# Kernel tuning notes

Measured on AMD Instinct MI355X. Metric: run time of the kernel, lower is better.

Reference implementation:

```python
import jax, jax.numpy as jnp
import numpy as np

N_HEAD = 12

def setup_inputs() -> dict:
    key = jax.random.key(0)
    k1, k2, k3 = jax.random.split(key, 3)
    B, T, C = 8, 1024, 768
    x = jax.random.normal(k1, (B, T, C), dtype=jnp.float32)
    # Linear weights stored as [in, out] so y = x @ W + b (same math as torch Linear)
    w_attn = jax.random.normal(k2, (C, 3 * C), dtype=jnp.float32) * (1.0 / np.sqrt(C))
    b_attn = jnp.zeros((3 * C,), dtype=jnp.float32)
    w_proj = jax.random.normal(k3, (C, C), dtype=jnp.float32) * (1.0 / np.sqrt(C))
    b_proj = jnp.zeros((C,), dtype=jnp.float32)
    return {"x": x, "w_attn": w_attn, "b_attn": b_attn, "w_proj": w_proj, "b_proj": b_proj}

def reference(x, w_attn, b_attn, w_proj, b_proj):
    B, T, C = x.shape
    H = N_HEAD
    D = C // H
    qkv = x @ w_attn + b_attn                        # [B,T,3C]
    q, k, v = jnp.split(qkv, 3, axis=-1)             # each [B,T,C]
    q = q.reshape(B, T, H, D).transpose(0, 2, 1, 3)  # [B,H,T,D]
    k = k.reshape(B, T, H, D).transpose(0, 2, 1, 3)
    v = v.reshape(B, T, H, D).transpose(0, 2, 1, 3)
    scale = 1.0 / jnp.sqrt(jnp.asarray(D, dtype=x.dtype))
    att = jnp.einsum('bhqd,bhkd->bhqk', q, k) * scale  # [B,H,T,T]
    causal = jnp.tril(jnp.ones((T, T), dtype=bool))    # [T,T]
    att = jnp.where(causal[None, None], att, jnp.asarray(-jnp.inf, dtype=att.dtype))
    att = jax.nn.softmax(att, axis=-1)
    out = jnp.einsum('bhqk,bhkd->bhqd', att, v)        # [B,H,T,D]
    out = out.transpose(0, 2, 1, 3).reshape(B, T, C)
    return out @ w_proj + b_proj
```

## Files before the change

kernel.cpp:

```cpp
#include <hip/hip_runtime.h>
#include <hip/hip_bf16.h>
#include <cmath>

#define B_ 8
#define T_ 1024
#define C_ 768
#define H_ 12
#define D_ 64
#define N3C 2304
#define M_ 8192

typedef __bf16 bf16x8 __attribute__((ext_vector_type(8)));
typedef float  f32x4  __attribute__((ext_vector_type(4)));

typedef const __attribute__((address_space(1))) void* gptr_t;
typedef __attribute__((address_space(3))) void* lptr_t;

#define LOG2E 1.44269504088896f

__device__ __forceinline__ bf16x8 cvt_bf16x8(const float4& a, const float4& b) {
    bf16x8 r;
    r[0] = (__bf16)a.x; r[1] = (__bf16)a.y; r[2] = (__bf16)a.z; r[3] = (__bf16)a.w;
    r[4] = (__bf16)b.x; r[5] = (__bf16)b.y; r[6] = (__bf16)b.z; r[7] = (__bf16)b.w;
    return r;
}

__global__ __launch_bounds__(256) void prepass(const float* __restrict__ x,
                                               __bf16* __restrict__ xb,
                                               const float* __restrict__ wa,
                                               __bf16* __restrict__ wat,
                                               const float* __restrict__ wp,
                                               __bf16* __restrict__ wpt) {
    __shared__ float tile[32][33];
    const int bx = blockIdx.x, tid = threadIdx.x;
    if (bx < 3072) {
        int i = (bx * 256 + tid) * 8;
        float4 a = *(const float4*)&x[i];
        float4 b = *(const float4*)&x[i + 4];
        *(bf16x8*)&xb[i] = cvt_bf16x8(a, b);
        return;
    }
    const float* w;
    __bf16* wt;
    int K, N, n0, k0;
    if (bx < 4800) {
        int bb = bx - 3072;
        w = wa; wt = wat; K = 768; N = 2304;
        n0 = (bb % 72) * 32; k0 = (bb / 72) * 32;
    } else {
        int bb = bx - 4800;
        w = wp; wt = wpt; K = 768; N = 768;
        n0 = (bb % 24) * 32; k0 = (bb / 24) * 32;
    }
    int tx = tid & 31, ty = tid >> 5;
#pragma unroll
    for (int i = 0; i < 4; i++)
        tile[ty + i * 8][tx] = w[(size_t)(k0 + ty + i * 8) * N + n0 + tx];
    __syncthreads();
#pragma unroll
    for (int i = 0; i < 4; i++)
        wt[(size_t)(n0 + ty + i * 8) * K + k0 + tx] = (__bf16)tile[tx][ty + i * 8];
}

__global__ __launch_bounds__(256) void qkv_gemm_mfma(const __bf16* __restrict__ A,
                                                     const __bf16* __restrict__ Bt,
                                                     const float* __restrict__ bias,
                                                     __bf16* __restrict__ qb,
                                                     __bf16* __restrict__ kb,
                                                     __bf16* __restrict__ vbt) {
    __shared__ __bf16 smem[128 * 136];
    __bf16* As = smem;
    __bf16* Bs = smem + 128 * 64;
    const int tid = threadIdx.x;
    const int wave = tid >> 6, lane = tid & 63;
    const int lane15 = lane & 15, quad = lane >> 4;
    const int bid = blockIdx.x;
    const int m0 = ((bid & 7) * 8 + ((bid >> 3) & 7)) * 128;
    const int n0 = (bid >> 6) * 128;
    const int wm = (wave >> 1) * 64, wn = (wave & 1) * 64;
    f32x4 acc[4][4] = {};

    for (int k0 = 0; k0 < 768; k0 += 64) {
#pragma unroll
        for (int r = 0; r < 4; ++r) {
            int p = r * 256 + tid;
            int mrow = p >> 3, csw = p & 7;
            int ksrc = (csw ^ (mrow & 7)) * 8;
            __builtin_amdgcn_global_load_lds(
                (gptr_t)(A + (size_t)(m0 + mrow) * 768 + k0 + ksrc),
                (lptr_t)(As + (r * 256 + wave * 64) * 8), 16, 0, 0);
            __builtin_amdgcn_global_load_lds(
                (gptr_t)(Bt + (size_t)(n0 + mrow) * 768 + k0 + ksrc),
                (lptr_t)(Bs + (r * 256 + wave * 64) * 8), 16, 0, 0);
        }
        __syncthreads();
#pragma unroll
        for (int ks = 0; ks < 2; ++ks) {
            bf16x8 af[4], bf[4];
#pragma unroll
            for (int mt = 0; mt < 4; ++mt) {
                int m = wm + mt * 16 + lane15;
                int csw = (ks * 4 + quad) ^ (m & 7);
                af[mt] = *(const bf16x8*)(As + m * 64 + csw * 8);
            }
#pragma unroll
            for (int nt = 0; nt < 4; ++nt) {
                int n = wn + nt * 16 + lane15;
                int csw = (ks * 4 + quad) ^ (n & 7);
                bf[nt] = *(const bf16x8*)(Bs + n * 64 + csw * 8);
            }
#pragma unroll
            for (int mt = 0; mt < 4; ++mt)
#pragma unroll
                for (int nt = 0; nt < 4; ++nt)
                    acc[mt][nt] = __builtin_amdgcn_mfma_f32_16x16x32_bf16(af[mt], bf[nt], acc[mt][nt], 0, 0, 0);
        }
        __syncthreads();
    }

    if (n0 < 1536) {
        const bool isq = (n0 < 768);
        const float sc = isq ? (0.125f * LOG2E) : 1.0f;
#pragma unroll
        for (int nt = 0; nt < 4; ++nt) {
            int n = n0 + wn + nt * 16 + lane15;
            int rem = isq ? n : (n - 768);
            int h = rem >> 6;
            int d = n & 63;
            float bv = bias[n];
            __bf16* dst = isq ? qb : kb;
#pragma unroll
            for (int mt = 0; mt < 4; ++mt) {
#pragma unroll
                for (int reg = 0; reg < 4; ++reg) {
                    int mr = m0 + wm + mt * 16 + quad * 4 + reg;
                    int bb = mr >> 10, t = mr & 1023;
                    dst[(((size_t)bb * H_ + h) * T_ + t) * D_ + d] =
                        (__bf16)((acc[mt][nt][reg] + bv) * sc);
                }
            }
        }
    } else {
        __bf16* vls = smem;
#pragma unroll
        for (int nt = 0; nt < 4; ++nt) {
            int nl = wn + nt * 16 + lane15;
            float bv = bias[n0 + nl];
#pragma unroll
            for (int mt = 0; mt < 4; ++mt)
#pragma unroll
                for (int reg = 0; reg < 4; ++reg)
                    vls[nl * 136 + wm + mt * 16 + quad * 4 + reg] =
                        (__bf16)(acc[mt][nt][reg] + bv);
        }
        __syncthreads();
        int nl = tid >> 1;
        int t0 = (tid & 1) * 64;
        int n = n0 + nl;
        int h = (n - 1536) >> 6;
        int d = n & 63;
        int bb = m0 >> 10, tg = (m0 & 1023) + t0;
        __bf16* dst = vbt + (((size_t)bb * H_ + h) * D_ + d) * T_ + tg;
        const __bf16* srcl = vls + nl * 136 + t0;
#pragma unroll
        for (int c = 0; c < 8; ++c)
            *(bf16x8*)(dst + c * 8) = *(const bf16x8*)(srcl + c * 8);
    }
}

__global__ __launch_bounds__(256) void proj_gemm_mfma(const __bf16* __restrict__ A,
                                                      const __bf16* __restrict__ Bt,
                                                      const float* __restrict__ bias,
                                                      float* __restrict__ out) {
    __shared__ __bf16 As[128 * 64];
    __shared__ __bf16 Bs[64 * 64];
    const int tid = threadIdx.x;
    const int wave = tid >> 6, lane = tid & 63;
    const int lane15 = lane & 15, quad = lane >> 4;
    const int bid = blockIdx.x;
    const int m0 = ((bid & 7) * 8 + ((bid >> 3) & 7)) * 128;
    const int n0 = (bid >> 6) * 64;
    const int wm = wave * 32;
    f32x4 acc[2][4] = {};

    for (int k0 = 0; k0 < 768; k0 += 64) {
#pragma unroll
        for (int r = 0; r < 4; ++r) {
            int p = r * 256 + tid;
            int mrow = p >> 3, csw = p & 7;
            int ksrc = (csw ^ (mrow & 7)) * 8;
            __builtin_amdgcn_global_load_lds(
                (gptr_t)(A + (size_t)(m0 + mrow) * 768 + k0 + ksrc),
                (lptr_t)(As + (r * 256 + wave * 64) * 8), 16, 0, 0);
        }
#pragma unroll
        for (int r = 0; r < 2; ++r) {
            int p = r * 256 + tid;
            int nrow = p >> 3, csw = p & 7;
            int ksrc = (csw ^ (nrow & 7)) * 8;
            __builtin_amdgcn_global_load_lds(
                (gptr_t)(Bt + (size_t)(n0 + nrow) * 768 + k0 + ksrc),
                (lptr_t)(Bs + (r * 256 + wave * 64) * 8), 16, 0, 0);
        }
        __syncthreads();
#pragma unroll
        for (int ks = 0; ks < 2; ++ks) {
            bf16x8 af[2], bf[4];
#pragma unroll
            for (int mt = 0; mt < 2; ++mt) {
                int m = wm + mt * 16 + lane15;
                int csw = (ks * 4 + quad) ^ (m & 7);
                af[mt] = *(const bf16x8*)(As + m * 64 + csw * 8);
            }
#pragma unroll
            for (int nt = 0; nt < 4; ++nt) {
                int n = nt * 16 + lane15;
                int csw = (ks * 4 + quad) ^ (n & 7);
                bf[nt] = *(const bf16x8*)(Bs + n * 64 + csw * 8);
            }
#pragma unroll
            for (int mt = 0; mt < 2; ++mt)
#pragma unroll
                for (int nt = 0; nt < 4; ++nt)
                    acc[mt][nt] = __builtin_amdgcn_mfma_f32_16x16x32_bf16(af[mt], bf[nt], acc[mt][nt], 0, 0, 0);
        }
        __syncthreads();
    }

#pragma unroll
    for (int nt = 0; nt < 4; ++nt) {
        int n = n0 + nt * 16 + lane15;
        float bv = bias[n];
#pragma unroll
        for (int mt = 0; mt < 2; ++mt) {
#pragma unroll
            for (int reg = 0; reg < 4; ++reg) {
                int mr = m0 + wm + mt * 16 + quad * 4 + reg;
                out[(size_t)mr * C_ + n] = acc[mt][nt][reg] + bv;
            }
        }
    }
}

__global__ __launch_bounds__(256) void attn_mfma(const __bf16* __restrict__ qb,
                                                 const __bf16* __restrict__ kb,
                                                 const __bf16* __restrict__ vbt,
                                                 __bf16* __restrict__ ao) {
    __shared__ __bf16 Ks[2][64 * 64];
    __shared__ __bf16 Vts[2][64 * 64];
    __shared__ __bf16 Ps[4 * 32 * 72];

    const int tid = threadIdx.x;
    const int wave = tid >> 6, lane = tid & 63;
    const int lane15 = lane & 15, quad = lane >> 4;
    const int bh = blockIdx.x;
    const int qt = 7 - blockIdx.y;
    const int b = bh / H_, h = bh % H_;
    const int q0 = qt * 128;

    const __bf16* Kb = kb + (size_t)bh * T_ * D_;
    const __bf16* Vb = vbt + (size_t)bh * D_ * T_;
    __bf16* Pw = Ps + wave * 32 * 72;

    bf16x8 qf[2][2];
#pragma unroll
    for (int g = 0; g < 2; ++g) {
        const __bf16* qrow = qb + ((size_t)bh * T_ + q0 + wave * 32 + g * 16 + lane15) * D_ + quad * 8;
        qf[g][0] = *(const bf16x8*)qrow;
        qf[g][1] = *(const bf16x8*)(qrow + 32);
    }

    f32x4 o[2][4] = {};
    float lsum[2][4] = {};

    const int kunits = 2 * qt + 2;

#define STAGE(KU, BUF)                                                             \
    {                                                                              \
        const int k0s = (KU) * 64;                                                 \
        _Pragma("unroll")                                                          \
        for (int r = 0; r < 2; ++r) {                                              \
            int p = r * 256 + tid;                                                 \
            int row = p >> 3, c = p & 7;                                           \
            int cs = (c ^ (row & 7)) * 8;                                          \
            __builtin_amdgcn_global_load_lds(                                      \
                (gptr_t)(Kb + (size_t)(k0s + row) * D_ + cs),                      \
                (lptr_t)(&Ks[BUF][0] + (r * 256 + wave * 64) * 8), 16, 0, 0);      \
            __builtin_amdgcn_global_load_lds(                                      \
                (gptr_t)(Vb + (size_t)row * T_ + k0s + cs),                        \
                (lptr_t)(&Vts[BUF][0] + (r * 256 + wave * 64) * 8), 16, 0, 0);     \
        }                                                                          \
    }

    STAGE(0, 0);

    for (int ku = 0; ku < kunits; ++ku) {
        __syncthreads();
        if (ku + 1 < kunits) STAGE(ku + 1, (ku + 1) & 1);
        const __bf16* Kc = &Ks[ku & 1][0];
        const __bf16* Vc = &Vts[ku & 1][0];
        const int k0 = ku * 64;

        f32x4 s[2][4];
#pragma unroll
        for (int kt = 0; kt < 4; ++kt) {
            int row = kt * 16 + lane15;
            bf16x8 kf0 = *(const bf16x8*)(Kc + row * 64 + ((quad) ^ (row & 7)) * 8);
            bf16x8 kf1 = *(const bf16x8*)(Kc + row * 64 + ((4 + quad) ^ (row & 7)) * 8);
#pragma unroll
            for (int g = 0; g < 2; ++g) {
                f32x4 t = {};
                t = __builtin_amdgcn_mfma_f32_16x16x32_bf16(qf[g][0], kf0, t, 0, 0, 0);
                t = __builtin_amdgcn_mfma_f32_16x16x32_bf16(qf[g][1], kf1, t, 0, 0, 0);
                s[g][kt] = t;
            }
        }

        const bool diag = (ku >= 2 * qt);
#pragma unroll
        for (int g = 0; g < 2; ++g) {
#pragma unroll
            for (int kt = 0; kt < 4; ++kt) {
                int col = k0 + kt * 16 + lane15;
#pragma unroll
                for (int r = 0; r < 4; ++r) {
                    float p = __builtin_amdgcn_exp2f(s[g][kt][r]);
                    if (diag) {
                        int qrow = q0 + wave * 32 + g * 16 + quad * 4 + r;
                        if (col > qrow) p = 0.f;
                    }
                    lsum[g][r] += p;
                    Pw[(g * 16 + quad * 4 + r) * 72 + kt * 16 + lane15] = (__bf16)p;
                }
            }
        }

        bf16x8 vf[4][2];
#pragma unroll
        for (int dt = 0; dt < 4; ++dt) {
            int row = dt * 16 + lane15;
#pragma unroll
            for (int half = 0; half < 2; ++half)
                vf[dt][half] = *(const bf16x8*)(Vc + row * 64 + ((half * 4 + quad) ^ (row & 7)) * 8);
        }
#pragma unroll
        for (int g = 0; g < 2; ++g) {
#pragma unroll
            for (int half = 0; half < 2; ++half) {
                bf16x8 pf = *(const bf16x8*)(Pw + (g * 16 + lane15) * 72 + half * 32 + quad * 8);
#pragma unroll
                for (int dt = 0; dt < 4; ++dt)
                    o[g][dt] = __builtin_amdgcn_mfma_f32_16x16x32_bf16(pf, vf[dt][half], o[g][dt], 0, 0, 0);
            }
        }
    }

#pragma unroll
    for (int g = 0; g < 2; ++g) {
        float inv[4];
#pragma unroll
        for (int r = 0; r < 4; ++r) {
            float ls = lsum[g][r];
            ls += __shfl_xor(ls, 1);
            ls += __shfl_xor(ls, 2);
            ls += __shfl_xor(ls, 4);
            ls += __shfl_xor(ls, 8);
            inv[r] = 1.0f / ls;
        }
#pragma unroll
        for (int dt = 0; dt < 4; ++dt) {
#pragma unroll
            for (int r = 0; r < 4; ++r) {
                int t = q0 + wave * 32 + g * 16 + quad * 4 + r;
                ao[((size_t)(b * T_ + t)) * C_ + h * 64 + dt * 16 + lane15] =
                    (__bf16)(o[g][dt][r] * inv[r]);
            }
        }
    }
}

extern "C" void kernel_launch(void* const* d_in, const int* in_sizes, int n_in,
                              void* d_out, int out_size, void* d_ws, size_t ws_size,
                              hipStream_t stream) {
    const float* x = (const float*)d_in[0];
    const float* w_attn = (const float*)d_in[1];
    const float* b_attn = (const float*)d_in[2];
    const float* w_proj = (const float*)d_in[3];
    const float* b_proj = (const float*)d_in[4];
    float* out = (float*)d_out;

    __bf16* xb = (__bf16*)d_ws;
    __bf16* wat = xb + (size_t)M_ * C_;
    __bf16* wpt = wat + (size_t)N3C * C_;
    __bf16* qb = wpt + (size_t)C_ * C_;
    __bf16* kb = qb + (size_t)96 * T_ * D_;
    __bf16* vbt = kb + (size_t)96 * T_ * D_;
    __bf16* ao = vbt + (size_t)96 * T_ * D_;

    prepass<<<5376, 256, 0, stream>>>(x, xb, w_attn, wat, w_proj, wpt);
    qkv_gemm_mfma<<<1152, 256, 0, stream>>>(xb, wat, b_attn, qb, kb, vbt);
    attn_mfma<<<dim3(96, 8), 256, 0, stream>>>(qb, kb, vbt, ao);
    proj_gemm_mfma<<<768, 256, 0, stream>>>(ao, wpt, b_proj, out);
}
```

Baseline: 188.9 us.

## Double-buffer GEMM K-loops and vectorize attention P stores via permuted V layout

The QKV and projection GEMMs now use two LDS buffers. The next K-chunk is prefetched with global_load_lds while the current one is computed, which drops one __syncthreads per iteration and hides global load latency. In attention, the per-element bf16 writes of P to LDS become one 4-wide vector store per row. That permutes the key order within each 64-key block, so the V-transpose epilogue of the QKV GEMM is changed to write V in the matching permuted order. The cost is double the LDS in the GEMMs, which may lower occupancy, and a scalar gather in the V epilogue.

```diff
diff --git a/kernel.cpp b/kernel.cpp
--- a/kernel.cpp
+++ b/kernel.cpp
@@ -10,6 +10,7 @@
 #define N3C 2304
 #define M_ 8192
 
+typedef __bf16 bf16x4 __attribute__((ext_vector_type(4)));
 typedef __bf16 bf16x8 __attribute__((ext_vector_type(8)));
 typedef float  f32x4  __attribute__((ext_vector_type(4)));
 
@@ -68,9 +69,7 @@
                                                      __bf16* __restrict__ qb,
                                                      __bf16* __restrict__ kb,
                                                      __bf16* __restrict__ vbt) {
-    __shared__ __bf16 smem[128 * 136];
-    __bf16* As = smem;
-    __bf16* Bs = smem + 128 * 64;
+    __shared__ __bf16 smem[2][2][128 * 64];
     const int tid = threadIdx.x;
     const int wave = tid >> 6, lane = tid & 63;
     const int lane15 = lane & 15, quad = lane >> 4;
@@ -80,20 +79,29 @@
     const int wm = (wave >> 1) * 64, wn = (wave & 1) * 64;
     f32x4 acc[4][4] = {};
 
-    for (int k0 = 0; k0 < 768; k0 += 64) {
-#pragma unroll
-        for (int r = 0; r < 4; ++r) {
-            int p = r * 256 + tid;
-            int mrow = p >> 3, csw = p & 7;
-            int ksrc = (csw ^ (mrow & 7)) * 8;
-            __builtin_amdgcn_global_load_lds(
-                (gptr_t)(A + (size_t)(m0 + mrow) * 768 + k0 + ksrc),
-                (lptr_t)(As + (r * 256 + wave * 64) * 8), 16, 0, 0);
-            __builtin_amdgcn_global_load_lds(
-                (gptr_t)(Bt + (size_t)(n0 + mrow) * 768 + k0 + ksrc),
-                (lptr_t)(Bs + (r * 256 + wave * 64) * 8), 16, 0, 0);
-        }
+#define QSTAGE(KC, BUF)                                                             \
+    {                                                                               \
+        const int k0s = (KC) * 64;                                                  \
+        _Pragma("unroll")                                                           \
+        for (int r = 0; r < 4; ++r) {                                               \
+            int p = r * 256 + tid;                                                  \
+            int mrow = p >> 3, csw = p & 7;                                         \
+            int ksrc = (csw ^ (mrow & 7)) * 8;                                      \
+            __builtin_amdgcn_global_load_lds(                                       \
+                (gptr_t)(A + (size_t)(m0 + mrow) * 768 + k0s + ksrc),               \
+                (lptr_t)(&smem[BUF][0][0] + (r * 256 + wave * 64) * 8), 16, 0, 0);  \
+            __builtin_amdgcn_global_load_lds(                                       \
+                (gptr_t)(Bt + (size_t)(n0 + mrow) * 768 + k0s + ksrc),              \
+                (lptr_t)(&smem[BUF][1][0] + (r * 256 + wave * 64) * 8), 16, 0, 0);  \
+        }                                                                           \
+    }
+
+    QSTAGE(0, 0);
+    for (int kc = 0; kc < 12; ++kc) {
         __syncthreads();
+        if (kc + 1 < 12) QSTAGE(kc + 1, (kc + 1) & 1);
+        const __bf16* As = &smem[kc & 1][0][0];
+        const __bf16* Bs = &smem[kc & 1][1][0];
 #pragma unroll
         for (int ks = 0; ks < 2; ++ks) {
             bf16x8 af[4], bf[4];
@@ -115,8 +123,8 @@
                 for (int nt = 0; nt < 4; ++nt)
                     acc[mt][nt] = __builtin_amdgcn_mfma_f32_16x16x32_bf16(af[mt], bf[nt], acc[mt][nt], 0, 0, 0);
         }
-        __syncthreads();
-    }
+    }
+    __syncthreads();
 
     if (n0 < 1536) {
         const bool isq = (n0 < 768);
@@ -141,7 +149,7 @@
             }
         }
     } else {
-        __bf16* vls = smem;
+        __bf16* vls = &smem[0][0][0];
 #pragma unroll
         for (int nt = 0; nt < 4; ++nt) {
             int nl = wn + nt * 16 + lane15;
@@ -163,8 +171,15 @@
         __bf16* dst = vbt + (((size_t)bb * H_ + h) * D_ + d) * T_ + tg;
         const __bf16* srcl = vls + nl * 136 + t0;
 #pragma unroll
-        for (int c = 0; c < 8; ++c)
-            *(bf16x8*)(dst + c * 8) = *(const bf16x8*)(srcl + c * 8);
+        for (int c = 0; c < 8; ++c) {
+            bf16x8 v;
+#pragma unroll
+            for (int i = 0; i < 8; ++i) {
+                int s = c * 8 + i;
+                v[i] = srcl[(s & 3) * 16 + (s >> 2)];
+            }
+            *(bf16x8*)(dst + c * 8) = v;
+        }
     }
 }
 
@@ -172,8 +187,8 @@
                                                       const __bf16* __restrict__ Bt,
                                                       const float* __restrict__ bias,
                                                       float* __restrict__ out) {
-    __shared__ __bf16 As[128 * 64];
-    __shared__ __bf16 Bs[64 * 64];
+    __shared__ __bf16 As[2][128 * 64];
+    __shared__ __bf16 Bs[2][64 * 64];
     const int tid = threadIdx.x;
     const int wave = tid >> 6, lane = tid & 63;
     const int lane15 = lane & 15, quad = lane >> 4;
@@ -183,26 +198,35 @@
     const int wm = wave * 32;
     f32x4 acc[2][4] = {};
 
-    for (int k0 = 0; k0 < 768; k0 += 64) {
-#pragma unroll
-        for (int r = 0; r < 4; ++r) {
-            int p = r * 256 + tid;
-            int mrow = p >> 3, csw = p & 7;
-            int ksrc = (csw ^ (mrow & 7)) * 8;
-            __builtin_amdgcn_global_load_lds(
-                (gptr_t)(A + (size_t)(m0 + mrow) * 768 + k0 + ksrc),
-                (lptr_t)(As + (r * 256 + wave * 64) * 8), 16, 0, 0);
-        }
-#pragma unroll
-        for (int r = 0; r < 2; ++r) {
-            int p = r * 256 + tid;
-            int nrow = p >> 3, csw = p & 7;
-            int ksrc = (csw ^ (nrow & 7)) * 8;
-            __builtin_amdgcn_global_load_lds(
-                (gptr_t)(Bt + (size_t)(n0 + nrow) * 768 + k0 + ksrc),
-                (lptr_t)(Bs + (r * 256 + wave * 64) * 8), 16, 0, 0);
-        }
+#define PSTAGE(KC, BUF)                                                             \
+    {                                                                               \
+        const int k0s = (KC) * 64;                                                  \
+        _Pragma("unroll")                                                           \
+        for (int r = 0; r < 4; ++r) {                                               \
+            int p = r * 256 + tid;                                                  \
+            int mrow = p >> 3, csw = p & 7;                                         \
+            int ksrc = (csw ^ (mrow & 7)) * 8;                                      \
+            __builtin_amdgcn_global_load_lds(                                       \
+                (gptr_t)(A + (size_t)(m0 + mrow) * 768 + k0s + ksrc),               \
+                (lptr_t)(&As[BUF][0] + (r * 256 + wave * 64) * 8), 16, 0, 0);       \
+        }                                                                           \
+        _Pragma("unroll")                                                           \
+        for (int r = 0; r < 2; ++r) {                                               \
+            int p = r * 256 + tid;                                                  \
+            int nrow = p >> 3, csw = p & 7;                                         \
+            int ksrc = (csw ^ (nrow & 7)) * 8;                                      \
+            __builtin_amdgcn_global_load_lds(                                       \
+                (gptr_t)(Bt + (size_t)(n0 + nrow) * 768 + k0s + ksrc),              \
+                (lptr_t)(&Bs[BUF][0] + (r * 256 + wave * 64) * 8), 16, 0, 0);       \
+        }                                                                           \
+    }
+
+    PSTAGE(0, 0);
+    for (int kc = 0; kc < 12; ++kc) {
         __syncthreads();
+        if (kc + 1 < 12) PSTAGE(kc + 1, (kc + 1) & 1);
+        const __bf16* Ac = &As[kc & 1][0];
+        const __bf16* Bc = &Bs[kc & 1][0];
 #pragma unroll
         for (int ks = 0; ks < 2; ++ks) {
             bf16x8 af[2], bf[4];
@@ -210,13 +234,13 @@
             for (int mt = 0; mt < 2; ++mt) {
                 int m = wm + mt * 16 + lane15;
                 int csw = (ks * 4 + quad) ^ (m & 7);
-                af[mt] = *(const bf16x8*)(As + m * 64 + csw * 8);
+                af[mt] = *(const bf16x8*)(Ac + m * 64 + csw * 8);
             }
 #pragma unroll
             for (int nt = 0; nt < 4; ++nt) {
                 int n = nt * 16 + lane15;
                 int csw = (ks * 4 + quad) ^ (n & 7);
-                bf[nt] = *(const bf16x8*)(Bs + n * 64 + csw * 8);
+                bf[nt] = *(const bf16x8*)(Bc + n * 64 + csw * 8);
             }
 #pragma unroll
             for (int mt = 0; mt < 2; ++mt)
@@ -224,7 +248,6 @@
                 for (int nt = 0; nt < 4; ++nt)
                     acc[mt][nt] = __builtin_amdgcn_mfma_f32_16x16x32_bf16(af[mt], bf[nt], acc[mt][nt], 0, 0, 0);
         }
-        __syncthreads();
     }
 
 #pragma unroll
@@ -275,7 +298,7 @@
 
     const int kunits = 2 * qt + 2;
 
-#define STAGE(KU, BUF)                                                             \
+#define ASTAGE(KU, BUF)                                                            \
     {                                                                              \
         const int k0s = (KU) * 64;                                                 \
         _Pragma("unroll")                                                          \
@@ -292,11 +315,11 @@
         }                                                                          \
     }
 
-    STAGE(0, 0);
+    ASTAGE(0, 0);
 
     for (int ku = 0; ku < kunits; ++ku) {
         __syncthreads();
-        if (ku + 1 < kunits) STAGE(ku + 1, (ku + 1) & 1);
+        if (ku + 1 < kunits) ASTAGE(ku + 1, (ku + 1) & 1);
         const __bf16* Kc = &Ks[ku & 1][0];
         const __bf16* Vc = &Vts[ku & 1][0];
         const int k0 = ku * 64;
@@ -320,18 +343,20 @@
 #pragma unroll
         for (int g = 0; g < 2; ++g) {
 #pragma unroll
-            for (int kt = 0; kt < 4; ++kt) {
-                int col = k0 + kt * 16 + lane15;
-#pragma unroll
-                for (int r = 0; r < 4; ++r) {
+            for (int r = 0; r < 4; ++r) {
+                bf16x4 pk;
+#pragma unroll
+                for (int kt = 0; kt < 4; ++kt) {
+                    int col = k0 + kt * 16 + lane15;
                     float p = __builtin_amdgcn_exp2f(s[g][kt][r]);
                     if (diag) {
                         int qrow = q0 + wave * 32 + g * 16 + quad * 4 + r;
                         if (col > qrow) p = 0.f;
                     }
                     lsum[g][r] += p;
-                    Pw[(g * 16 + quad * 4 + r) * 72 + kt * 16 + lane15] = (__bf16)p;
+                    pk[kt] = (__bf16)p;
                 }
+                *(bf16x4*)(Pw + (g * 16 + quad * 4 + r) * 72 + lane15 * 4) = pk;
             }
         }
 
```

Measured after the change: 175.9 us. 1.07x faster.
